# Optimization experiments

Measured on AMD Instinct MI355X. Metric: run time of the kernel, lower is better.

## Reference

```python
import jax, jax.numpy as jnp
import numpy as np

DIM = 192
WS = 8
HEADS = 6
HD = DIM // HEADS
RECON_W = 0.1
EPS = 1e-6


def setup_inputs() -> dict:
    key = jax.random.key(0)
    ks = jax.random.split(key, 10)
    d = DIM

    def rn(k, shape, scale=0.02):
        return jax.random.normal(k, shape, jnp.float32) * scale

    return {
        "x": jax.random.normal(ks[0], (4, d, 224, 224), jnp.float32),
        "w_pre1": rn(ks[1], (d, d)), "b_pre1": jnp.zeros((d,), jnp.float32),
        "w_dw": rn(ks[2], (d, 3, 3)), "b_dw": jnp.zeros((d,), jnp.float32),
        "ln_g": jnp.ones((d,), jnp.float32), "ln_b": jnp.zeros((d,), jnp.float32),
        "w_qkv": rn(ks[3], (d, 3 * d)), "b_qkv": jnp.zeros((3 * d,), jnp.float32),
        "w_proj": rn(ks[4], (d, d)), "b_proj": jnp.zeros((d,), jnp.float32),
        "w_g1": rn(ks[5], (d, 4 * d)), "b_g1": jnp.zeros((4 * d,), jnp.float32),
        "w_g2": rn(ks[6], (4 * d, d)), "b_g2": jnp.zeros((d,), jnp.float32),
        "w_rec": rn(ks[7], (d, d)), "b_rec": jnp.zeros((d,), jnp.float32),
    }


def _forward(x, w_pre1, b_pre1, w_dw, b_dw, ln_g, ln_b, w_qkv, b_qkv,
             w_proj, b_proj, w_g1, b_g1, w_g2, b_g2, w_rec, b_rec):
    B, C, H, W = x.shape
    ws, nh, hd = WS, HEADS, HD
    shortcut = x

    # preprocess: 1x1 conv then depthwise 3x3 conv (padding=1)
    f = jnp.einsum('bchw,oc->bohw', x, w_pre1) + b_pre1[None, :, None, None]
    f = jax.lax.conv_general_dilated(
        f, w_dw[:, None, :, :], (1, 1), 'SAME',
        feature_group_count=C,
        dimension_numbers=('NCHW', 'OIHW', 'NCHW')) + b_dw[None, :, None, None]

    # LayerNorm2d: LN over channel dim
    f = f.transpose(0, 2, 3, 1)  # BHWC
    mu = f.mean(-1, keepdims=True)
    var = f.var(-1, keepdims=True)
    f = (f - mu) / jnp.sqrt(var + EPS) * ln_g + ln_b

    # window partition (H, W divisible by ws -> no padding needed)
    nH, nW = H // ws, W // ws
    p = f.reshape(B, nH, ws, nW, ws, C).transpose(0, 1, 3, 2, 4, 5)
    p = p.reshape(B * nH * nW, ws * ws, C)  # [N, T, C]
    N, T, _ = p.shape

    # qkv + windowed multi-head attention
    qkv = p @ w_qkv + b_qkv
    q, k, v = jnp.split(qkv, 3, axis=-1)
    qh = q.reshape(N, T, nh, hd)
    kh = k.reshape(N, T, nh, hd)
    vh = v.reshape(N, T, nh, hd)
    scale = hd ** (-0.5)
    attn = jnp.einsum('nqhd,nkhd->nhqk', qh, kh) * scale
    attn = jax.nn.softmax(attn, axis=-1)
    out_attn = jnp.einsum('nhqk,nkhd->nqhd', attn, vh).reshape(N, T, C)

    # GMLP on v (dropout is identity in eval); torch GELU is exact erf form
    g = jax.nn.gelu(v @ w_g1 + b_g1, approximate=False) @ w_g2 + b_g2

    fused = (out_attn * g) @ w_proj + b_proj

    # recon head + L1 loss vs detached window tokens
    recon = fused @ w_rec + b_rec
    recon_loss = jnp.mean(jnp.abs(recon - jax.lax.stop_gradient(p))) * RECON_W

    # window reverse
    out = fused.reshape(B, nH, nW, ws, ws, C).transpose(0, 5, 1, 3, 2, 4)
    out = out.reshape(B, C, H, W)
    return out + shortcut, recon_loss


def reference(x, w_pre1, b_pre1, w_dw, b_dw, ln_g, ln_b, w_qkv, b_qkv,
              w_proj, b_proj, w_g1, b_g1, w_g2, b_g2, w_rec, b_rec):
    return _forward(x, w_pre1, b_pre1, w_dw, b_dw, ln_g, ln_b, w_qkv, b_qkv,
                    w_proj, b_proj, w_g1, b_g1, w_g2, b_g2, w_rec, b_rec)
```

## Files before the change

kernel.cpp:

```cpp
#include <hip/hip_runtime.h>
#include <hip/hip_bf16.h>
#include <math.h>

#define BATCH 4
#define CDIM 192
#define HDIM 224
#define WDIM 224
#define HWSZ (HDIM * WDIM)
#define NWH 28
#define NWIN (BATCH * NWH * NWH)
#define TOK 64
#define MTOK (NWIN * TOK)
#define HEADS 6
#define C3 (3 * CDIM)
#define C4 (4 * CDIM)
#define IMGSZ (BATCH * CDIM * HWSZ)
#define ATTN_SCALE 0.17677669529663687f
#define LN_EPS 1e-6f
#define PBP 200

typedef __attribute__((ext_vector_type(8))) short bfrag;
typedef __attribute__((ext_vector_type(4))) float f32x4;

__device__ __forceinline__ float bf2f(unsigned short u) {
    union { unsigned int i; float f; } v; v.i = ((unsigned int)u) << 16; return v.f;
}
__device__ __forceinline__ unsigned short f2bf(float f) {
    union { unsigned int i; float f; } v; v.f = f;
    unsigned int r = (v.i + 0x7FFFu + ((v.i >> 16) & 1u)) >> 16;
    return (unsigned short)r;
}
__device__ __forceinline__ float gelu_erf(float x) {
    float z = fabsf(x) * 0.70710678118654752f;
    float t = __fdividef(1.0f, 1.0f + 0.3275911f * z);
    float poly = t * (0.254829592f + t * (-0.284496736f +
                 t * (1.421413741f + t * (-1.453152027f + t * 1.061405429f))));
    float erfv = 1.0f - poly * __expf(-z * z);
    erfv = (x < 0.f) ? -erfv : erfv;
    return 0.5f * x * (1.0f + erfv);
}
__device__ __forceinline__ void gload16(void* lds, const void* g) {
    __builtin_amdgcn_global_load_lds(
        (const __attribute__((address_space(1))) void*)g,
        (__attribute__((address_space(3))) void*)lds, 16, 0, 0);
}

__launch_bounds__(256)
__global__ void prep_weights_kernel(const float* __restrict__ w_qkv,
                                    const float* __restrict__ w_g1,
                                    const float* __restrict__ w_g2,
                                    const float* __restrict__ w_proj,
                                    const float* __restrict__ w_rec,
                                    ushort* __restrict__ WqkvT,
                                    ushort* __restrict__ W1T,
                                    ushort* __restrict__ W2C,
                                    ushort* __restrict__ WpT,
                                    ushort* __restrict__ WrT) {
    int idx = blockIdx.x * 256 + threadIdx.x;
    if (idx < 576 * 192) {
        int n = idx / 192, k = idx % 192;
        WqkvT[idx] = f2bf(w_qkv[(size_t)k * C3 + n]);
    }
    if (idx < 768 * 192) {
        int n = idx / 192, k = idx % 192;
        W1T[idx] = f2bf(w_g1[(size_t)k * C4 + n]);
    }
    if (idx < 192 * 768) {
        int hc = idx / 12288, rem = idx % 12288;
        int n = rem / 64, kloc = rem & 63;
        W2C[idx] = f2bf(w_g2[(size_t)(hc * 64 + kloc) * CDIM + n]);
    }
    if (idx < 192 * 192) {
        int n = idx / 192, k = idx % 192;
        WpT[idx] = f2bf(w_proj[(size_t)k * CDIM + n]);
        WrT[idx] = f2bf(w_rec[(size_t)k * CDIM + n]);
    }
}

__launch_bounds__(256)
__global__ void conv1x1_kernel(const float* __restrict__ x,
                               const float* __restrict__ w1,
                               const float* __restrict__ b1,
                               float* __restrict__ f1) {
    __shared__ __align__(16) float As[16][68];
    __shared__ __align__(16) float Bs[16][64];
    const int tid = threadIdx.x;
    const int p0 = blockIdx.x * 64;
    const int m0 = blockIdx.y * 64;
    const int b  = blockIdx.z;
    const int tm = tid >> 4, tn = tid & 15;
    const int mload = tid >> 2, kload = (tid & 3) * 4;
    const int kw = tid >> 4, nw = (tid & 15) * 4;
    float acc[4][4] = {};
    const float* xb = x + (size_t)b * CDIM * HWSZ;
    for (int k0 = 0; k0 < CDIM; k0 += 16) {
        float4 av = *(const float4*)&w1[(size_t)(m0 + mload) * CDIM + k0 + kload];
        float4 bv = *(const float4*)&xb[(size_t)(k0 + kw) * HWSZ + p0 + nw];
        __syncthreads();
        As[kload + 0][mload] = av.x;
        As[kload + 1][mload] = av.y;
        As[kload + 2][mload] = av.z;
        As[kload + 3][mload] = av.w;
        *(float4*)&Bs[kw][nw] = bv;
        __syncthreads();
#pragma unroll
        for (int kk = 0; kk < 16; ++kk) {
            float a[4], bb[4];
            *(float4*)a  = *(const float4*)&As[kk][tm * 4];
            *(float4*)bb = *(const float4*)&Bs[kk][tn * 4];
#pragma unroll
            for (int i = 0; i < 4; ++i)
#pragma unroll
                for (int j = 0; j < 4; ++j) acc[i][j] += a[i] * bb[j];
        }
    }
    float* outb = f1 + (size_t)b * CDIM * HWSZ;
#pragma unroll
    for (int i = 0; i < 4; ++i) {
        int m = m0 + tm * 4 + i;
        float bias = b1[m];
        float4 o = make_float4(acc[i][0] + bias, acc[i][1] + bias,
                               acc[i][2] + bias, acc[i][3] + bias);
        *(float4*)&outb[(size_t)m * HWSZ + p0 + tn * 4] = o;
    }
}

__launch_bounds__(256)
__global__ void dwconv_kernel(const float* __restrict__ f1,
                              const float* __restrict__ w_dw,
                              const float* __restrict__ b_dw,
                              float* __restrict__ f2) {
    unsigned int idx = blockIdx.x * 256u + threadIdx.x;
    int w = idx % WDIM;
    unsigned int r = idx / WDIM;
    int h = r % HDIM;
    unsigned int bc = r / HDIM;
    int c = bc % CDIM;
    const float* base = f1 + (size_t)bc * HWSZ;
    const float* wd = w_dw + c * 9;
    float acc = b_dw[c];
#pragma unroll
    for (int ky = 0; ky < 3; ++ky) {
        int hy = h + ky - 1;
        if (hy < 0 || hy >= HDIM) continue;
#pragma unroll
        for (int kx = 0; kx < 3; ++kx) {
            int wx = w + kx - 1;
            if (wx < 0 || wx >= WDIM) continue;
            acc += base[hy * WDIM + wx] * wd[ky * 3 + kx];
        }
    }
    f2[idx] = acc;
}

__launch_bounds__(256)
__global__ void ln_part_kernel(const float* __restrict__ f2,
                               const float* __restrict__ ln_g,
                               const float* __restrict__ ln_b,
                               ushort* __restrict__ pb) {
    __shared__ float T[CDIM][33];
    __shared__ float Rs[8][32], Rs2[8][32];
    __shared__ float Mu[32], Rsig[32];
    const int tid = threadIdx.x;
    const int wt = blockIdx.x, h = blockIdx.y, b = blockIdx.z;
    const int w0 = wt * 32;
    const size_t rowbase = (size_t)b * CDIM * HWSZ + (size_t)h * WDIM + w0;
    for (int idx = tid; idx < CDIM * 32; idx += 256) {
        int c = idx >> 5, j = idx & 31;
        T[c][j] = f2[rowbase + (size_t)c * HWSZ + j];
    }
    __syncthreads();
    {
        int j = tid & 31, q = tid >> 5;
        float s = 0.f, s2 = 0.f;
#pragma unroll
        for (int i = 0; i < 24; ++i) {
            float v = T[q * 24 + i][j];
            s += v; s2 += v * v;
        }
        Rs[q][j] = s; Rs2[q][j] = s2;
    }
    __syncthreads();
    if (tid < 32) {
        float s = 0.f, s2 = 0.f;
#pragma unroll
        for (int q = 0; q < 8; ++q) { s += Rs[q][tid]; s2 += Rs2[q][tid]; }
        float mu = s * (1.0f / CDIM);
        float var = s2 * (1.0f / CDIM) - mu * mu;
        Mu[tid] = mu;
        Rsig[tid] = rsqrtf(var + LN_EPS);
    }
    __syncthreads();
    const int l = tid & 63;
    const int jo = tid >> 6;
    for (int it = 0; it < 8; ++it) {
        int j = it * 4 + jo;
        int w = w0 + j;
        size_t token = ((size_t)(b * NWH + (h >> 3)) * NWH + (w >> 3)) * TOK
                       + ((h & 7) * 8 + (w & 7));
        float mu = Mu[j], rs = Rsig[j];
#pragma unroll
        for (int rep = 0; rep < 3; ++rep) {
            int c = l + rep * 64;
            pb[token * PBP + c] = f2bf((T[c][j] - mu) * rs * ln_g[c] + ln_b[c]);
        }
    }
}

__launch_bounds__(256, 3)
__global__ void attn_mfma_kernel(const ushort* __restrict__ pb,
                                 const ushort* __restrict__ WqkvT,
                                 const float* __restrict__ b_qkv,
                                 float* __restrict__ oa) {
    __shared__ __align__(16) ushort Pt[64 * PBP];
    __shared__ __align__(16) ushort Qb[64 * 40];
    __shared__ __align__(16) ushort Kb[64 * 40];
    __shared__ __align__(16) ushort Vt[32 * 72];
    __shared__ __align__(16) ushort Pbf[64 * 72];
    const int tid = threadIdx.x;
    const int lane = tid & 63, wave = tid >> 6;
    const int quad = lane >> 4, l16 = lane & 15;
    const int m0 = wave * 16;
    const size_t tok0 = (size_t)blockIdx.x * 64;

    {
        char* PtB = (char*)Pt;
        const char* src = (const char*)(pb + tok0 * PBP);
#pragma unroll
        for (int c = 0; c < 6; ++c) {
            int base = (wave * 6 + c) * 1024;
            gload16(PtB + base, src + base + lane * 16);
        }
        if (wave == 0) gload16(PtB + 24576, src + 24576 + lane * 16);
    }
    __syncthreads();

    for (int h = 0; h < HEADS; ++h) {
        const ushort* baseQ = WqkvT + (size_t)(h * 32) * 192;
        const ushort* baseK = WqkvT + (size_t)(192 + h * 32) * 192;
        const ushort* baseV = WqkvT + (size_t)(384 + h * 32) * 192;
        f32x4 acc[6];
#pragma unroll
        for (int t = 0; t < 6; ++t) acc[t] = (f32x4){0.f, 0.f, 0.f, 0.f};
#pragma unroll
        for (int kk = 0; kk < 6; ++kk) {
            const int ko = kk * 32 + quad * 8;
            bfrag b0 = *(const bfrag*)&baseQ[(size_t)l16 * 192 + ko];
            bfrag b1 = *(const bfrag*)&baseQ[(size_t)(16 + l16) * 192 + ko];
            bfrag b2 = *(const bfrag*)&baseK[(size_t)l16 * 192 + ko];
            bfrag b3 = *(const bfrag*)&baseK[(size_t)(16 + l16) * 192 + ko];
            bfrag b4 = *(const bfrag*)&baseV[(size_t)l16 * 192 + ko];
            bfrag b5 = *(const bfrag*)&baseV[(size_t)(16 + l16) * 192 + ko];
            bfrag a  = *(const bfrag*)&Pt[(m0 + l16) * PBP + ko];
            __builtin_amdgcn_s_setprio(1);
            acc[0] = __builtin_amdgcn_mfma_f32_16x16x32_bf16(a, b0, acc[0], 0, 0, 0);
            acc[1] = __builtin_amdgcn_mfma_f32_16x16x32_bf16(a, b1, acc[1], 0, 0, 0);
            acc[2] = __builtin_amdgcn_mfma_f32_16x16x32_bf16(a, b2, acc[2], 0, 0, 0);
            acc[3] = __builtin_amdgcn_mfma_f32_16x16x32_bf16(a, b3, acc[3], 0, 0, 0);
            acc[4] = __builtin_amdgcn_mfma_f32_16x16x32_bf16(a, b4, acc[4], 0, 0, 0);
            acc[5] = __builtin_amdgcn_mfma_f32_16x16x32_bf16(a, b5, acc[5], 0, 0, 0);
            __builtin_amdgcn_s_setprio(0);
        }
#pragma unroll
        for (int t = 0; t < 2; ++t) {
            float bq = b_qkv[h * 32 + t * 16 + l16];
            float bk = b_qkv[192 + h * 32 + t * 16 + l16];
            float bv = b_qkv[384 + h * 32 + t * 16 + l16];
#pragma unroll
            for (int reg = 0; reg < 4; ++reg) {
                int row = m0 + quad * 4 + reg;
                Qb[row * 40 + t * 16 + l16] = f2bf((acc[t][reg] + bq) * ATTN_SCALE);
                Kb[row * 40 + t * 16 + l16] = f2bf(acc[t + 2][reg] + bk);
                Vt[(t * 16 + l16) * 72 + row] = f2bf(acc[t + 4][reg] + bv);
            }
        }
        __syncthreads();

        f32x4 s[4];
        {
            bfrag aq = *(const bfrag*)&Qb[(m0 + l16) * 40 + quad * 8];
            bfrag k0 = *(const bfrag*)&Kb[(l16) * 40 + quad * 8];
            bfrag k1 = *(const bfrag*)&Kb[(16 + l16) * 40 + quad * 8];
            bfrag k2 = *(const bfrag*)&Kb[(32 + l16) * 40 + quad * 8];
            bfrag k3 = *(const bfrag*)&Kb[(48 + l16) * 40 + quad * 8];
            __builtin_amdgcn_s_setprio(1);
            s[0] = __builtin_amdgcn_mfma_f32_16x16x32_bf16(
                aq, k0, (f32x4){0.f, 0.f, 0.f, 0.f}, 0, 0, 0);
            s[1] = __builtin_amdgcn_mfma_f32_16x16x32_bf16(
                aq, k1, (f32x4){0.f, 0.f, 0.f, 0.f}, 0, 0, 0);
            s[2] = __builtin_amdgcn_mfma_f32_16x16x32_bf16(
                aq, k2, (f32x4){0.f, 0.f, 0.f, 0.f}, 0, 0, 0);
            s[3] = __builtin_amdgcn_mfma_f32_16x16x32_bf16(
                aq, k3, (f32x4){0.f, 0.f, 0.f, 0.f}, 0, 0, 0);
            __builtin_amdgcn_s_setprio(0);
        }
#pragma unroll
        for (int reg = 0; reg < 4; ++reg) {
            float mx = fmaxf(fmaxf(s[0][reg], s[1][reg]), fmaxf(s[2][reg], s[3][reg]));
            mx = fmaxf(mx, __shfl_xor(mx, 1));
            mx = fmaxf(mx, __shfl_xor(mx, 2));
            mx = fmaxf(mx, __shfl_xor(mx, 4));
            mx = fmaxf(mx, __shfl_xor(mx, 8));
            float e[4], sum = 0.f;
#pragma unroll
            for (int t = 0; t < 4; ++t) { e[t] = __expf(s[t][reg] - mx); sum += e[t]; }
            sum += __shfl_xor(sum, 1);
            sum += __shfl_xor(sum, 2);
            sum += __shfl_xor(sum, 4);
            sum += __shfl_xor(sum, 8);
            float inv = 1.0f / sum;
            int row = m0 + quad * 4 + reg;
#pragma unroll
            for (int t = 0; t < 4; ++t)
                Pbf[row * 72 + t * 16 + l16] = f2bf(e[t] * inv);
        }
        __syncthreads();

        f32x4 o[2];
        o[0] = (f32x4){0.f, 0.f, 0.f, 0.f};
        o[1] = (f32x4){0.f, 0.f, 0.f, 0.f};
#pragma unroll
        for (int kk = 0; kk < 2; ++kk) {
            bfrag a  = *(const bfrag*)&Pbf[(m0 + l16) * 72 + kk * 32 + quad * 8];
            bfrag v0 = *(const bfrag*)&Vt[(l16) * 72 + kk * 32 + quad * 8];
            bfrag v1 = *(const bfrag*)&Vt[(16 + l16) * 72 + kk * 32 + quad * 8];
            __builtin_amdgcn_s_setprio(1);
            o[0] = __builtin_amdgcn_mfma_f32_16x16x32_bf16(a, v0, o[0], 0, 0, 0);
            o[1] = __builtin_amdgcn_mfma_f32_16x16x32_bf16(a, v1, o[1], 0, 0, 0);
            __builtin_amdgcn_s_setprio(0);
        }
#pragma unroll
        for (int t = 0; t < 2; ++t) {
            int col = h * 32 + t * 16 + l16;
#pragma unroll
            for (int reg = 0; reg < 4; ++reg) {
                int row = m0 + quad * 4 + reg;
                oa[(tok0 + row) * (size_t)CDIM + col] = o[t][reg];
            }
        }
        __syncthreads();
    }
}

__launch_bounds__(256)
__global__ void gmlp_mfma_kernel(const ushort* __restrict__ pb,
                                 const ushort* __restrict__ WvT,
                                 const float* __restrict__ b_qkv,
                                 const ushort* __restrict__ W1T,
                                 const float* __restrict__ b_g1,
                                 const ushort* __restrict__ W2C,
                                 const float* __restrict__ b_g2,
                                 float* __restrict__ a_io) {
    __shared__ __align__(16) ushort Ab[64 * PBP];
    __shared__ __align__(16) ushort Wb[12288];
    __shared__ __align__(16) ushort Hb[64 * 72];
    const int tid = threadIdx.x;
    const int lane = tid & 63, wave = tid >> 6;
    const int quad = lane >> 4, l16 = lane & 15;
    const int m0 = wave * 16;
    const int sw = (l16 & 7) << 3;
    const size_t tok0 = (size_t)blockIdx.x * 64;

    int srcA[6], srcB[6], dst6[6];
#pragma unroll
    for (int c = 0; c < 6; ++c) {
        int P = (wave * 6 + c) * 1024 + lane * 16;
        dst6[c] = (wave * 6 + c) * 1024;
        int rA = P / 384;
        int mA = P - rA * 384;
        srcA[c] = rA * 384 + (mA ^ ((rA & 7) << 4));
        srcB[c] = P ^ (((P >> 7) & 7) << 4);
    }
    char* WbB = (char*)Wb;
    char* AbB = (char*)Ab;

#define ISSUE_W(SRC, OFFS)                                                    \
    _Pragma("unroll")                                                         \
    for (int c = 0; c < 6; ++c)                                               \
        gload16(WbB + dst6[c], (const char*)(SRC) + OFFS[c]);

    {
        const char* src = (const char*)(pb + tok0 * PBP);
#pragma unroll
        for (int c = 0; c < 6; ++c)
            gload16(AbB + dst6[c], src + dst6[c] + lane * 16);
        if (wave == 0) gload16(AbB + 24576, src + 24576 + lane * 16);
    }
    ISSUE_W(WvT, srcA);
    __syncthreads();

    f32x4 vacc[12];
#pragma unroll
    for (int i = 0; i < 12; ++i) vacc[i] = (f32x4){0.f, 0.f, 0.f, 0.f};

#define COMPUTE_K192(ACC, BASEI)                                              \
    _Pragma("unroll")                                                         \
    for (int kk = 0; kk < 6; ++kk) {                                          \
        bfrag a = *(const bfrag*)&Ab[(m0 + l16) * PBP + kk * 32 + quad * 8];  \
        _Pragma("unroll")                                                     \
        for (int t = 0; t < 4; ++t) {                                         \
            bfrag b = *(const bfrag*)&Wb[(t * 16 + l16) * 192                 \
                                         + ((kk * 32 + quad * 8) ^ sw)];      \
            ACC[(BASEI) + t] = __builtin_amdgcn_mfma_f32_16x16x32_bf16(       \
                a, b, ACC[(BASEI) + t], 0, 0, 0);                             \
        }                                                                     \
    }

    COMPUTE_K192(vacc, 0);
    __syncthreads();
    ISSUE_W((const char*)WvT + 24576, srcA);
    __syncthreads();
    COMPUTE_K192(vacc, 4);
    __syncthreads();
    ISSUE_W((const char*)WvT + 49152, srcA);
    __syncthreads();
    COMPUTE_K192(vacc, 8);
#pragma unroll
    for (int i = 0; i < 12; ++i) {
        int n = i * 16 + l16;
        float bias = b_qkv[384 + n];
#pragma unroll
        for (int reg = 0; reg < 4; ++reg) {
            int r = m0 + quad * 4 + reg;
            Ab[r * PBP + n] = f2bf(vacc[i][reg] + bias);
        }
    }
    __syncthreads();
    ISSUE_W(W1T, srcA);
    __syncthreads();

    f32x4 acc2[12];
#pragma unroll
    for (int i = 0; i < 12; ++i) acc2[i] = (f32x4){0.f, 0.f, 0.f, 0.f};
    for (int hc = 0; hc < 12; ++hc) {
        f32x4 acc1[4];
#pragma unroll
        for (int t = 0; t < 4; ++t) acc1[t] = (f32x4){0.f, 0.f, 0.f, 0.f};
        COMPUTE_K192(acc1, 0);
#pragma unroll
        for (int t = 0; t < 4; ++t) {
            int n = t * 16 + l16;
            float bb = b_g1[hc * 64 + n];
#pragma unroll
            for (int reg = 0; reg < 4; ++reg) {
                float xv = acc1[t][reg] + bb;
                Hb[(m0 + quad * 4 + reg) * 72 + n] = f2bf(gelu_erf(xv));
            }
        }
        __syncthreads();
        ISSUE_W((const char*)W2C + (size_t)hc * 24576, srcB);
        __syncthreads();
#pragma unroll
        for (int kk = 0; kk < 2; ++kk) {
            bfrag a = *(const bfrag*)&Hb[(m0 + l16) * 72 + kk * 32 + quad * 8];
#pragma unroll
            for (int t = 0; t < 12; ++t) {
                bfrag b = *(const bfrag*)&Wb[(t * 16 + l16) * 64
                                             + ((kk * 32 + quad * 8) ^ sw)];
                acc2[t] = __builtin_amdgcn_mfma_f32_16x16x32_bf16(a, b, acc2[t], 0, 0, 0);
            }
        }
        if (hc < 11) {
            __syncthreads();
            ISSUE_W((const char*)W1T + (size_t)(hc + 1) * 24576, srcA);
            __syncthreads();
        }
    }
#pragma unroll
    for (int t = 0; t < 12; ++t) {
        int c = t * 16 + l16;
        float bg = b_g2[c];
#pragma unroll
        for (int reg = 0; reg < 4; ++reg) {
            size_t idx = (tok0 + m0 + quad * 4 + reg) * CDIM + c;
            a_io[idx] *= (acc2[t][reg] + bg);
        }
    }
#undef ISSUE_W
#undef COMPUTE_K192
}

__launch_bounds__(256)
__global__ void proj_recon_kernel(const ushort* __restrict__ WpT,
                                  const float* __restrict__ b_proj,
                                  const ushort* __restrict__ WrT,
                                  const float* __restrict__ b_rec,
                                  const ushort* __restrict__ pb,
                                  float* __restrict__ a_io,
                                  float* __restrict__ loss) {
    __shared__ __align__(16) ushort Tb[64 * PBP];
    __shared__ __align__(16) ushort Wb[12288];
    __shared__ float red[256];
    const int tid = threadIdx.x;
    const int lane = tid & 63, wave = tid >> 6;
    const int quad = lane >> 4, l16 = lane & 15;
    const int m0 = wave * 16;
    const int sw = (l16 & 7) << 3;
    const size_t tok0 = (size_t)blockIdx.x * 64;

    int srcA[6], dst6[6];
#pragma unroll
    for (int c = 0; c < 6; ++c) {
        int P = (wave * 6 + c) * 1024 + lane * 16;
        dst6[c] = (wave * 6 + c) * 1024;
        int rA = P / 384;
        int mA = P - rA * 384;
        srcA[c] = rA * 384 + (mA ^ ((rA & 7) << 4));
    }
    char* WbB = (char*)Wb;

#define PR_ISSUE(SRC)                                                         \
    _Pragma("unroll")                                                         \
    for (int c = 0; c < 6; ++c)                                               \
        gload16(WbB + dst6[c], (const char*)(SRC) + srcA[c]);
#define PR_COMPUTE(ACC, BASEI)                                                \
    _Pragma("unroll")                                                         \
    for (int kk = 0; kk < 6; ++kk) {                                          \
        bfrag a = *(const bfrag*)&Tb[(m0 + l16) * PBP + kk * 32 + quad * 8];  \
        _Pragma("unroll")                                                     \
        for (int t = 0; t < 4; ++t) {                                         \
            bfrag b = *(const bfrag*)&Wb[(t * 16 + l16) * 192                 \
                                         + ((kk * 32 + quad * 8) ^ sw)];      \
            ACC[(BASEI) + t] = __builtin_amdgcn_mfma_f32_16x16x32_bf16(       \
                a, b, ACC[(BASEI) + t], 0, 0, 0);                             \
        }                                                                     \
    }

    PR_ISSUE(WpT);
    for (int i4 = tid * 4; i4 < 64 * 192; i4 += 1024) {
        float4 v = *(const float4*)&a_io[tok0 * CDIM + i4];
        int r = i4 / 192, c = i4 - r * 192;
        ushort u[4] = { f2bf(v.x), f2bf(v.y), f2bf(v.z), f2bf(v.w) };
        *(uint2*)&Tb[r * PBP + c] = *(uint2*)u;
    }
    __syncthreads();

    f32x4 facc[12];
#pragma unroll
    for (int i = 0; i < 12; ++i) facc[i] = (f32x4){0.f, 0.f, 0.f, 0.f};
    PR_COMPUTE(facc, 0);
    __syncthreads();
    PR_ISSUE((const char*)WpT + 24576);
    __syncthreads();
    PR_COMPUTE(facc, 4);
    __syncthreads();
    PR_ISSUE((const char*)WpT + 49152);
    __syncthreads();
    PR_COMPUTE(facc, 8);
#pragma unroll
    for (int i = 0; i < 12; ++i) {
        int n = i * 16 + l16;
        float bp = b_proj[n];
#pragma unroll
        for (int reg = 0; reg < 4; ++reg) {
            int r = m0 + quad * 4 + reg;
            float fv = facc[i][reg] + bp;
            a_io[(tok0 + r) * (size_t)CDIM + n] = fv;
            Tb[r * PBP + n] = f2bf(fv);
        }
    }
    __syncthreads();
    PR_ISSUE(WrT);
    __syncthreads();

    f32x4 racc[12];
#pragma unroll
    for (int i = 0; i < 12; ++i) racc[i] = (f32x4){0.f, 0.f, 0.f, 0.f};
    PR_COMPUTE(racc, 0);
    __syncthreads();
    PR_ISSUE((const char*)WrT + 24576);
    __syncthreads();
    PR_COMPUTE(racc, 4);
    __syncthreads();
    PR_ISSUE((const char*)WrT + 49152);
    __syncthreads();
    PR_COMPUTE(racc, 8);

    float ls = 0.f;
#pragma unroll
    for (int i = 0; i < 12; ++i) {
        int n = i * 16 + l16;
        float br = b_rec[n];
#pragma unroll
        for (int reg = 0; reg < 4; ++reg) {
            int r = m0 + quad * 4 + reg;
            float rv = racc[i][reg] + br;
            ls += fabsf(rv - bf2f(pb[(tok0 + r) * PBP + n]));
        }
    }
    red[tid] = ls;
    __syncthreads();
    for (int s = 128; s > 0; s >>= 1) {
        if (tid < s) red[tid] += red[tid + s];
        __syncthreads();
    }
    if (tid == 0) atomicAdd(loss, red[0] * (0.1f / (float)IMGSZ));
#undef PR_ISSUE
#undef PR_COMPUTE
}

__launch_bounds__(256)
__global__ void reverse_res_kernel(const float* __restrict__ fused,
                                   const float* __restrict__ x,
                                   float* __restrict__ out) {
    __shared__ float T[CDIM][33];
    const int tid = threadIdx.x;
    const int wt = blockIdx.x, h = blockIdx.y, b = blockIdx.z;
    const int w0 = wt * 32;
    const int l = tid & 63, jo = tid >> 6;
    for (int it = 0; it < 8; ++it) {
        int j = it * 4 + jo;
        int w = w0 + j;
        size_t token = ((size_t)(b * NWH + (h >> 3)) * NWH + (w >> 3)) * TOK
                       + ((h & 7) * 8 + (w & 7));
#pragma unroll
        for (int rep = 0; rep < 3; ++rep) {
            int c = l + rep * 64;
            T[c][j] = fused[token * CDIM + c];
        }
    }
    __syncthreads();
    const size_t rowbase = (size_t)b * CDIM * HWSZ + (size_t)h * WDIM + w0;
    for (int idx = tid; idx < CDIM * 32; idx += 256) {
        int c = idx >> 5, j = idx & 31;
        size_t gp = rowbase + (size_t)c * HWSZ + j;
        out[gp] = T[c][j] + x[gp];
    }
}

extern "C" void kernel_launch(void* const* d_in, const int* in_sizes, int n_in,
                              void* d_out, int out_size, void* d_ws, size_t ws_size,
                              hipStream_t stream) {
    const float* x      = (const float*)d_in[0];
    const float* w_pre1 = (const float*)d_in[1];
    const float* b_pre1 = (const float*)d_in[2];
    const float* w_dw   = (const float*)d_in[3];
    const float* b_dw   = (const float*)d_in[4];
    const float* ln_g   = (const float*)d_in[5];
    const float* ln_b   = (const float*)d_in[6];
    const float* w_qkv  = (const float*)d_in[7];
    const float* b_qkv  = (const float*)d_in[8];
    const float* w_proj = (const float*)d_in[9];
    const float* b_proj = (const float*)d_in[10];
    const float* w_g1   = (const float*)d_in[11];
    const float* b_g1   = (const float*)d_in[12];
    const float* w_g2   = (const float*)d_in[13];
    const float* b_g2   = (const float*)d_in[14];
    const float* w_rec  = (const float*)d_in[15];
    const float* b_rec  = (const float*)d_in[16];

    float* OutR = (float*)d_out;
    float* loss = OutR + (size_t)IMGSZ;
    float* A    = (float*)d_ws;

    ushort* pb    = (ushort*)d_out;
    ushort* WqkvT = pb    + (size_t)MTOK * PBP;
    ushort* W1T   = WqkvT + 576 * 192;
    ushort* W2C   = W1T   + 768 * 192;
    ushort* WpT   = W2C   + 192 * 768;
    ushort* WrT   = WpT   + 192 * 192;
    ushort* WvT   = WqkvT + 384 * 192;

    hipMemsetAsync(loss, 0, sizeof(float), stream);

    conv1x1_kernel<<<dim3(HWSZ / 64, CDIM / 64, BATCH), 256, 0, stream>>>(
        x, w_pre1, b_pre1, OutR);
    dwconv_kernel<<<IMGSZ / 256, 256, 0, stream>>>(OutR, w_dw, b_dw, A);
    prep_weights_kernel<<<(768 * 192 + 255) / 256, 256, 0, stream>>>(
        w_qkv, w_g1, w_g2, w_proj, w_rec, WqkvT, W1T, W2C, WpT, WrT);
    ln_part_kernel<<<dim3(WDIM / 32, HDIM, BATCH), 256, 0, stream>>>(
        A, ln_g, ln_b, pb);
    attn_mfma_kernel<<<NWIN, 256, 0, stream>>>(pb, WqkvT, b_qkv, A);
    gmlp_mfma_kernel<<<MTOK / 64, 256, 0, stream>>>(
        pb, WvT, b_qkv, W1T, b_g1, W2C, b_g2, A);
    proj_recon_kernel<<<MTOK / 64, 256, 0, stream>>>(
        WpT, b_proj, WrT, b_rec, pb, A, loss);
    reverse_res_kernel<<<dim3(WDIM / 32, HDIM, BATCH), 256, 0, stream>>>(
        A, x, OutR);
}
```

Before: 1.599 ms.

## Fuse attention, GMLP and proj/recon into a single per-window mega kernel

```diff
diff --git a/kernel.cpp b/kernel.cpp
--- a/kernel.cpp
+++ b/kernel.cpp
@@ -207,34 +207,82 @@
     }
 }
 
-__launch_bounds__(256, 3)
-__global__ void attn_mfma_kernel(const ushort* __restrict__ pb,
-                                 const ushort* __restrict__ WqkvT,
-                                 const float* __restrict__ b_qkv,
-                                 float* __restrict__ oa) {
-    __shared__ __align__(16) ushort Pt[64 * PBP];
-    __shared__ __align__(16) ushort Qb[64 * 40];
-    __shared__ __align__(16) ushort Kb[64 * 40];
-    __shared__ __align__(16) ushort Vt[32 * 72];
-    __shared__ __align__(16) ushort Pbf[64 * 72];
+__launch_bounds__(256)
+__global__ void mega_kernel(const ushort* __restrict__ pb,
+                            const ushort* __restrict__ WqkvT,
+                            const float* __restrict__ b_qkv,
+                            const ushort* __restrict__ W1T,
+                            const float* __restrict__ b_g1,
+                            const ushort* __restrict__ W2C,
+                            const float* __restrict__ b_g2,
+                            const ushort* __restrict__ WpT,
+                            const float* __restrict__ b_proj,
+                            const ushort* __restrict__ WrT,
+                            const float* __restrict__ b_rec,
+                            float* __restrict__ Fout,
+                            float* __restrict__ loss) {
+    __shared__ __align__(16) ushort Ab[64 * PBP];
+    __shared__ __align__(16) ushort Blob[16896];
+    __shared__ float red[256];
+    ushort* Qb  = Blob;
+    ushort* Kb  = Blob + 2560;
+    ushort* Vt  = Blob + 5120;
+    ushort* Pbf = Blob + 7424;
+    ushort* Wb  = Blob;
+    ushort* Hb  = Blob + 12288;
+
     const int tid = threadIdx.x;
     const int lane = tid & 63, wave = tid >> 6;
     const int quad = lane >> 4, l16 = lane & 15;
     const int m0 = wave * 16;
+    const int sw = (l16 & 7) << 3;
     const size_t tok0 = (size_t)blockIdx.x * 64;
 
+    int srcA[6], srcB[6], dst6[6];
+#pragma unroll
+    for (int c = 0; c < 6; ++c) {
+        int P = (wave * 6 + c) * 1024 + lane * 16;
+        dst6[c] = (wave * 6 + c) * 1024;
+        int rA = P / 384;
+        int mA = P - rA * 384;
+        srcA[c] = rA * 384 + (mA ^ ((rA & 7) << 4));
+        srcB[c] = P ^ (((P >> 7) & 7) << 4);
+    }
+    char* WbB = (char*)Wb;
+    char* AbB = (char*)Ab;
+
+#define ISSUE_W(SRC, OFFS)                                                    \
+    _Pragma("unroll")                                                         \
+    for (int c = 0; c < 6; ++c)                                               \
+        gload16(WbB + dst6[c], (const char*)(SRC) + OFFS[c]);
+#define COMPUTE_K192(ACC, BASEI)                                              \
+    _Pragma("unroll")                                                         \
+    for (int kk = 0; kk < 6; ++kk) {                                          \
+        bfrag a = *(const bfrag*)&Ab[(m0 + l16) * PBP + kk * 32 + quad * 8];  \
+        _Pragma("unroll")                                                     \
+        for (int t = 0; t < 4; ++t) {                                         \
+            bfrag b = *(const bfrag*)&Wb[(t * 16 + l16) * 192                 \
+                                         + ((kk * 32 + quad * 8) ^ sw)];      \
+            ACC[(BASEI) + t] = __builtin_amdgcn_mfma_f32_16x16x32_bf16(       \
+                a, b, ACC[(BASEI) + t], 0, 0, 0);                             \
+        }                                                                     \
+    }
+
     {
-        char* PtB = (char*)Pt;
         const char* src = (const char*)(pb + tok0 * PBP);
 #pragma unroll
-        for (int c = 0; c < 6; ++c) {
-            int base = (wave * 6 + c) * 1024;
-            gload16(PtB + base, src + base + lane * 16);
-        }
-        if (wave == 0) gload16(PtB + 24576, src + 24576 + lane * 16);
-    }
-    __syncthreads();
-
+        for (int c = 0; c < 6; ++c)
+            gload16(AbB + dst6[c], src + dst6[c] + lane * 16);
+        if (wave == 0) gload16(AbB + 24576, src + 24576 + lane * 16);
+    }
+    __syncthreads();
+
+    f32x4 oacc[12];
+#pragma unroll
+    for (int i = 0; i < 12; ++i) oacc[i] = (f32x4){0.f, 0.f, 0.f, 0.f};
+    unsigned int vpk[12][2];
+
+#pragma unroll
     for (int h = 0; h < HEADS; ++h) {
         const ushort* baseQ = WqkvT + (size_t)(h * 32) * 192;
         const ushort* baseK = WqkvT + (size_t)(192 + h * 32) * 192;
@@ -251,7 +299,7 @@
             bfrag b3 = *(const bfrag*)&baseK[(size_t)(16 + l16) * 192 + ko];
             bfrag b4 = *(const bfrag*)&baseV[(size_t)l16 * 192 + ko];
             bfrag b5 = *(const bfrag*)&baseV[(size_t)(16 + l16) * 192 + ko];
-            bfrag a  = *(const bfrag*)&Pt[(m0 + l16) * PBP + ko];
+            bfrag a  = *(const bfrag*)&Ab[(m0 + l16) * PBP + ko];
             __builtin_amdgcn_s_setprio(1);
             acc[0] = __builtin_amdgcn_mfma_f32_16x16x32_bf16(a, b0, acc[0], 0, 0, 0);
             acc[1] = __builtin_amdgcn_mfma_f32_16x16x32_bf16(a, b1, acc[1], 0, 0, 0);
@@ -266,13 +314,18 @@
             float bq = b_qkv[h * 32 + t * 16 + l16];
             float bk = b_qkv[192 + h * 32 + t * 16 + l16];
             float bv = b_qkv[384 + h * 32 + t * 16 + l16];
+            ushort vb[4];
 #pragma unroll
             for (int reg = 0; reg < 4; ++reg) {
                 int row = m0 + quad * 4 + reg;
                 Qb[row * 40 + t * 16 + l16] = f2bf((acc[t][reg] + bq) * ATTN_SCALE);
                 Kb[row * 40 + t * 16 + l16] = f2bf(acc[t + 2][reg] + bk);
-                Vt[(t * 16 + l16) * 72 + row] = f2bf(acc[t + 4][reg] + bv);
+                ushort vv = f2bf(acc[t + 4][reg] + bv);
+                Vt[(t * 16 + l16) * 72 + row] = vv;
+                vb[reg] = vv;
             }
+            vpk[h * 2 + t][0] = (unsigned int)vb[0] | ((unsigned int)vb[1] << 16);
+            vpk[h * 2 + t][1] = (unsigned int)vb[2] | ((unsigned int)vb[3] << 16);
         }
         __syncthreads();
 
@@ -316,116 +369,29 @@
         }
         __syncthreads();
 
-        f32x4 o[2];
-        o[0] = (f32x4){0.f, 0.f, 0.f, 0.f};
-        o[1] = (f32x4){0.f, 0.f, 0.f, 0.f};
 #pragma unroll
         for (int kk = 0; kk < 2; ++kk) {
             bfrag a  = *(const bfrag*)&Pbf[(m0 + l16) * 72 + kk * 32 + quad * 8];
             bfrag v0 = *(const bfrag*)&Vt[(l16) * 72 + kk * 32 + quad * 8];
             bfrag v1 = *(const bfrag*)&Vt[(16 + l16) * 72 + kk * 32 + quad * 8];
             __builtin_amdgcn_s_setprio(1);
-            o[0] = __builtin_amdgcn_mfma_f32_16x16x32_bf16(a, v0, o[0], 0, 0, 0);
-            o[1] = __builtin_amdgcn_mfma_f32_16x16x32_bf16(a, v1, o[1], 0, 0, 0);
+            oacc[h * 2 + 0] = __builtin_amdgcn_mfma_f32_16x16x32_bf16(
+                a, v0, oacc[h * 2 + 0], 0, 0, 0);
+            oacc[h * 2 + 1] = __builtin_amdgcn_mfma_f32_16x16x32_bf16(
+                a, v1, oacc[h * 2 + 1], 0, 0, 0);
             __builtin_amdgcn_s_setprio(0);
         }
-#pragma unroll
-        for (int t = 0; t < 2; ++t) {
-            int col = h * 32 + t * 16 + l16;
-#pragma unroll
-            for (int reg = 0; reg < 4; ++reg) {
-                int row = m0 + quad * 4 + reg;
-                oa[(tok0 + row) * (size_t)CDIM + col] = o[t][reg];
-            }
-        }
-        __syncthreads();
-    }
-}
-
-__launch_bounds__(256)
-__global__ void gmlp_mfma_kernel(const ushort* __restrict__ pb,
-                                 const ushort* __restrict__ WvT,
-                                 const float* __restrict__ b_qkv,
-                                 const ushort* __restrict__ W1T,
-                                 const float* __restrict__ b_g1,
-                                 const ushort* __restrict__ W2C,
-                                 const float* __restrict__ b_g2,
-                                 float* __restrict__ a_io) {
-    __shared__ __align__(16) ushort Ab[64 * PBP];
-    __shared__ __align__(16) ushort Wb[12288];
-    __shared__ __align__(16) ushort Hb[64 * 72];
-    const int tid = threadIdx.x;
-    const int lane = tid & 63, wave = tid >> 6;
-    const int quad = lane >> 4, l16 = lane & 15;
-    const int m0 = wave * 16;
-    const int sw = (l16 & 7) << 3;
-    const size_t tok0 = (size_t)blockIdx.x * 64;
-
-    int srcA[6], srcB[6], dst6[6];
-#pragma unroll
-    for (int c = 0; c < 6; ++c) {
-        int P = (wave * 6 + c) * 1024 + lane * 16;
-        dst6[c] = (wave * 6 + c) * 1024;
-        int rA = P / 384;
-        int mA = P - rA * 384;
-        srcA[c] = rA * 384 + (mA ^ ((rA & 7) << 4));
-        srcB[c] = P ^ (((P >> 7) & 7) << 4);
-    }
-    char* WbB = (char*)Wb;
-    char* AbB = (char*)Ab;
-
-#define ISSUE_W(SRC, OFFS)                                                    \
-    _Pragma("unroll")                                                         \
-    for (int c = 0; c < 6; ++c)                                               \
-        gload16(WbB + dst6[c], (const char*)(SRC) + OFFS[c]);
-
-    {
-        const char* src = (const char*)(pb + tok0 * PBP);
-#pragma unroll
-        for (int c = 0; c < 6; ++c)
-            gload16(AbB + dst6[c], src + dst6[c] + lane * 16);
-        if (wave == 0) gload16(AbB + 24576, src + 24576 + lane * 16);
-    }
-    ISSUE_W(WvT, srcA);
-    __syncthreads();
-
-    f32x4 vacc[12];
-#pragma unroll
-    for (int i = 0; i < 12; ++i) vacc[i] = (f32x4){0.f, 0.f, 0.f, 0.f};
-
-#define COMPUTE_K192(ACC, BASEI)                                              \
-    _Pragma("unroll")                                                         \
-    for (int kk = 0; kk < 6; ++kk) {                                          \
-        bfrag a = *(const bfrag*)&Ab[(m0 + l16) * PBP + kk * 32 + quad * 8];  \
-        _Pragma("unroll")                                                     \
-        for (int t = 0; t < 4; ++t) {                                         \
-            bfrag b = *(const bfrag*)&Wb[(t * 16 + l16) * 192                 \
-                                         + ((kk * 32 + quad * 8) ^ sw)];      \
-            ACC[(BASEI) + t] = __builtin_amdgcn_mfma_f32_16x16x32_bf16(       \
-                a, b, ACC[(BASEI) + t], 0, 0, 0);                             \
-        }                                                                     \
-    }
-
-    COMPUTE_K192(vacc, 0);
-    __syncthreads();
-    ISSUE_W((const char*)WvT + 24576, srcA);
-    __syncthreads();
-    COMPUTE_K192(vacc, 4);
-    __syncthreads();
-    ISSUE_W((const char*)WvT + 49152, srcA);
-    __syncthreads();
-    COMPUTE_K192(vacc, 8);
+        __syncthreads();
+    }
+
 #pragma unroll
     for (int i = 0; i < 12; ++i) {
         int n = i * 16 + l16;
-        float bias = b_qkv[384 + n];
-#pragma unroll
-        for (int reg = 0; reg < 4; ++reg) {
-            int r = m0 + quad * 4 + reg;
-            Ab[r * PBP + n] = f2bf(vacc[i][reg] + bias);
-        }
-    }
-    __syncthreads();
+        Ab[(m0 + quad * 4 + 0) * PBP + n] = (ushort)(vpk[i][0] & 0xFFFF);
+        Ab[(m0 + quad * 4 + 1) * PBP + n] = (ushort)(vpk[i][0] >> 16);
+        Ab[(m0 + quad * 4 + 2) * PBP + n] = (ushort)(vpk[i][1] & 0xFFFF);
+        Ab[(m0 + quad * 4 + 3) * PBP + n] = (ushort)(vpk[i][1] >> 16);
+    }
     ISSUE_W(W1T, srcA);
     __syncthreads();
 
@@ -472,81 +438,26 @@
         float bg = b_g2[c];
 #pragma unroll
         for (int reg = 0; reg < 4; ++reg) {
-            size_t idx = (tok0 + m0 + quad * 4 + reg) * CDIM + c;
-            a_io[idx] *= (acc2[t][reg] + bg);
-        }
-    }
-#undef ISSUE_W
-#undef COMPUTE_K192
-}
-
-__launch_bounds__(256)
-__global__ void proj_recon_kernel(const ushort* __restrict__ WpT,
-                                  const float* __restrict__ b_proj,
-                                  const ushort* __restrict__ WrT,
-                                  const float* __restrict__ b_rec,
-                                  const ushort* __restrict__ pb,
-                                  float* __restrict__ a_io,
-                                  float* __restrict__ loss) {
-    __shared__ __align__(16) ushort Tb[64 * PBP];
-    __shared__ __align__(16) ushort Wb[12288];
-    __shared__ float red[256];
-    const int tid = threadIdx.x;
-    const int lane = tid & 63, wave = tid >> 6;
-    const int quad = lane >> 4, l16 = lane & 15;
-    const int m0 = wave * 16;
-    const int sw = (l16 & 7) << 3;
-    const size_t tok0 = (size_t)blockIdx.x * 64;
-
-    int srcA[6], dst6[6];
-#pragma unroll
-    for (int c = 0; c < 6; ++c) {
-        int P = (wave * 6 + c) * 1024 + lane * 16;
-        dst6[c] = (wave * 6 + c) * 1024;
-        int rA = P / 384;
-        int mA = P - rA * 384;
-        srcA[c] = rA * 384 + (mA ^ ((rA & 7) << 4));
-    }
-    char* WbB = (char*)Wb;
-
-#define PR_ISSUE(SRC)                                                         \
-    _Pragma("unroll")                                                         \
-    for (int c = 0; c < 6; ++c)                                               \
-        gload16(WbB + dst6[c], (const char*)(SRC) + srcA[c]);
-#define PR_COMPUTE(ACC, BASEI)                                                \
-    _Pragma("unroll")                                                         \
-    for (int kk = 0; kk < 6; ++kk) {                                          \
-        bfrag a = *(const bfrag*)&Tb[(m0 + l16) * PBP + kk * 32 + quad * 8];  \
-        _Pragma("unroll")                                                     \
-        for (int t = 0; t < 4; ++t) {                                         \
-            bfrag b = *(const bfrag*)&Wb[(t * 16 + l16) * 192                 \
-                                         + ((kk * 32 + quad * 8) ^ sw)];      \
-            ACC[(BASEI) + t] = __builtin_amdgcn_mfma_f32_16x16x32_bf16(       \
-                a, b, ACC[(BASEI) + t], 0, 0, 0);                             \
-        }                                                                     \
-    }
-
-    PR_ISSUE(WpT);
-    for (int i4 = tid * 4; i4 < 64 * 192; i4 += 1024) {
-        float4 v = *(const float4*)&a_io[tok0 * CDIM + i4];
-        int r = i4 / 192, c = i4 - r * 192;
-        ushort u[4] = { f2bf(v.x), f2bf(v.y), f2bf(v.z), f2bf(v.w) };
-        *(uint2*)&Tb[r * PBP + c] = *(uint2*)u;
-    }
+            int r = m0 + quad * 4 + reg;
+            Ab[r * PBP + c] = f2bf(oacc[t][reg] * (acc2[t][reg] + bg));
+        }
+    }
+    __syncthreads();
+    ISSUE_W(WpT, srcA);
     __syncthreads();
 
     f32x4 facc[12];
 #pragma unroll
     for (int i = 0; i < 12; ++i) facc[i] = (f32x4){0.f, 0.f, 0.f, 0.f};
-    PR_COMPUTE(facc, 0);
-    __syncthreads();
-    PR_ISSUE((const char*)WpT + 24576);
-    __syncthreads();
-    PR_COMPUTE(facc, 4);
-    __syncthreads();
-    PR_ISSUE((const char*)WpT + 49152);
-    __syncthreads();
-    PR_COMPUTE(facc, 8);
+    COMPUTE_K192(facc, 0);
+    __syncthreads();
+    ISSUE_W((const char*)WpT + 24576, srcA);
+    __syncthreads();
+    COMPUTE_K192(facc, 4);
+    __syncthreads();
+    ISSUE_W((const char*)WpT + 49152, srcA);
+    __syncthreads();
+    COMPUTE_K192(facc, 8);
 #pragma unroll
     for (int i = 0; i < 12; ++i) {
         int n = i * 16 + l16;
@@ -555,26 +466,26 @@
         for (int reg = 0; reg < 4; ++reg) {
             int r = m0 + quad * 4 + reg;
             float fv = facc[i][reg] + bp;
-            a_io[(tok0 + r) * (size_t)CDIM + n] = fv;
-            Tb[r * PBP + n] = f2bf(fv);
-        }
-    }
-    __syncthreads();
-    PR_ISSUE(WrT);
+            Fout[(tok0 + r) * (size_t)CDIM + n] = fv;
+            Ab[r * PBP + n] = f2bf(fv);
+        }
+    }
+    __syncthreads();
+    ISSUE_W(WrT, srcA);
     __syncthreads();
 
     f32x4 racc[12];
 #pragma unroll
     for (int i = 0; i < 12; ++i) racc[i] = (f32x4){0.f, 0.f, 0.f, 0.f};
-    PR_COMPUTE(racc, 0);
-    __syncthreads();
-    PR_ISSUE((const char*)WrT + 24576);
-    __syncthreads();
-    PR_COMPUTE(racc, 4);
-    __syncthreads();
-    PR_ISSUE((const char*)WrT + 49152);
-    __syncthreads();
-    PR_COMPUTE(racc, 8);
+    COMPUTE_K192(racc, 0);
+    __syncthreads();
+    ISSUE_W((const char*)WrT + 24576, srcA);
+    __syncthreads();
+    COMPUTE_K192(racc, 4);
+    __syncthreads();
+    ISSUE_W((const char*)WrT + 49152, srcA);
+    __syncthreads();
+    COMPUTE_K192(racc, 8);
 
     float ls = 0.f;
 #pragma unroll
@@ -595,8 +506,8 @@
         __syncthreads();
     }
     if (tid == 0) atomicAdd(loss, red[0] * (0.1f / (float)IMGSZ));
-#undef PR_ISSUE
-#undef PR_COMPUTE
+#undef ISSUE_W
+#undef COMPUTE_K192
 }
 
 __launch_bounds__(256)
@@ -659,7 +570,6 @@
     ushort* W2C   = W1T   + 768 * 192;
     ushort* WpT   = W2C   + 192 * 768;
     ushort* WrT   = WpT   + 192 * 192;
-    ushort* WvT   = WqkvT + 384 * 192;
 
     hipMemsetAsync(loss, 0, sizeof(float), stream);
 
@@ -670,11 +580,9 @@
         w_qkv, w_g1, w_g2, w_proj, w_rec, WqkvT, W1T, W2C, WpT, WrT);
     ln_part_kernel<<<dim3(WDIM / 32, HDIM, BATCH), 256, 0, stream>>>(
         A, ln_g, ln_b, pb);
-    attn_mfma_kernel<<<NWIN, 256, 0, stream>>>(pb, WqkvT, b_qkv, A);
-    gmlp_mfma_kernel<<<MTOK / 64, 256, 0, stream>>>(
-        pb, WvT, b_qkv, W1T, b_g1, W2C, b_g2, A);
-    proj_recon_kernel<<<MTOK / 64, 256, 0, stream>>>(
-        WpT, b_proj, WrT, b_rec, pb, A, loss);
+    mega_kernel<<<NWIN, 256, 0, stream>>>(
+        pb, WqkvT, b_qkv, W1T, b_g1, W2C, b_g2, WpT, b_proj, WrT, b_rec,
+        A, loss);
     reverse_res_kernel<<<dim3(WDIM / 32, HDIM, BATCH), 256, 0, stream>>>(
         A, x, OutR);
 }
```

Result: faster. 1.541 ms (-3.6%).
